# Kernel optimization log

Measured on AMD Instinct MI355X. Metric: run time of the kernel, lower is better.

The kernel has to match this reference:

```python
import jax, jax.numpy as jnp
import numpy as np

EMBED, PDIM, HEADS, FFN = 192, 96, 8, 384
HID = int(2 * FFN / 3)                        # 256
CH = [HID - (HID // 4) * 3] + [HID // 4] * 3  # [64, 64, 64, 64]
SCALES = [1, 3, 5, 7]
B, H, W = 8, 128, 128


def conv2d(x, w, b=None, pad=0, groups=1):
    out = jax.lax.conv_general_dilated(
        x, w, (1, 1), [(pad, pad), (pad, pad)],
        feature_group_count=groups,
        dimension_numbers=('NCHW', 'OIHW', 'NCHW'))
    return out if b is None else out + b[None, :, None, None]


def layer_norm(x, g, b, eps=1e-6):
    m = x.mean(-1, keepdims=True)
    v = ((x - m) ** 2).mean(-1, keepdims=True)
    return (x - m) * jax.lax.rsqrt(v + eps) * g + b


def batch_norm(x, g, b, m, v, eps=1e-5):
    # eval-mode BatchNorm2d with running stats
    inv = jax.lax.rsqrt(v + eps)
    return (x - m[None, :, None, None]) * (g * inv)[None, :, None, None] + b[None, :, None, None]


def block_forward(x, p):
    # --- pos: depthwise 3x3 residual ---
    xc = x.transpose(0, 3, 1, 2)  # NCHW
    xc = xc + conv2d(xc, p['pos_w'], p['pos_b'], pad=1, groups=EMBED)

    # --- retention (ATK_SPA) branch ---
    y = layer_norm(xc.transpose(0, 2, 3, 1), p['ln1_g'], p['ln1_b'])
    yc = y.transpose(0, 3, 1, 2)
    b, c, h, w = yc.shape
    x1, x2 = yc[:, :PDIM], yc[:, PDIM:]
    qkv = conv2d(conv2d(x1, p['qkv_w']), p['qkv_dw_w'], pad=1, groups=3 * PDIM)
    q, k, v = jnp.split(qkv, 3, axis=1)
    cph = PDIM // HEADS
    rs = lambda t: t.reshape(b, HEADS, cph, h * w)
    q, k, v = rs(q), rs(k), rs(v)
    q = q / jnp.maximum(jnp.linalg.norm(q, axis=-1, keepdims=True), 1e-12)
    k = k / jnp.maximum(jnp.linalg.norm(k, axis=-1, keepdims=True), 1e-12)
    attn = jnp.einsum('bhcn,bhdn->bhcd', q, k) * p['temperature']  # [b,heads,cph,cph]
    # dynamic top-k from gate (int() truncation -> floor, value is positive)
    g1 = jax.nn.relu(conv2d(yc, p['gate_w1'], p['gate_b1']))
    gate = jax.nn.sigmoid(conv2d(g1, p['gate_w2'], p['gate_b2']))
    dyn_k = jnp.floor(cph * gate.mean())
    # rank-based top-k mask == scatter of topk indices (jit-safe for dynamic k)
    ranks = jnp.argsort(jnp.argsort(-attn, axis=-1), axis=-1)
    mask = ranks.astype(attn.dtype) < dyn_k
    attn = jax.nn.softmax(jnp.where(mask, attn, -jnp.inf), axis=-1)
    out = jnp.einsum('bhcd,bhdn->bhcn', attn, v)
    # out1..out4 are identical; weighted sum == single matmul scaled
    out = out * (p['attn1'] + p['attn2'] + p['attn3'] + p['attn4'])
    out = out.reshape(b, PDIM, h, w)
    out = conv2d(jnp.concatenate([out, x2], axis=1), p['proj_w'])
    xc = xc + out

    # --- FFN (HSSFGN) branch ---
    z = layer_norm(xc.transpose(0, 2, 3, 1), p['ln2_g'], p['ln2_b'])
    zc = z.transpose(0, 3, 1, 2)
    v0 = batch_norm(jax.nn.gelu(conv2d(zc, p['fc1_w']), approximate=False),
                    p['bn1_g'], p['bn1_b'], p['bn1_m'], p['bn1_v'])
    parts = jnp.split(v0, np.cumsum(CH[:-1]).tolist(), axis=1)
    dws = [conv2d(parts[i], p['dw%d_w' % i], p['dw%d_b' % i],
                  pad=SCALES[i] // 2, groups=CH[i]) for i in range(4)]
    u = jnp.concatenate(dws, axis=1) + v0
    u = batch_norm(jax.nn.gelu(u, approximate=False),
                   p['bn2_g'], p['bn2_b'], p['bn2_m'], p['bn2_v'])
    u = u * v0
    u = batch_norm(conv2d(u, p['fc2_w']),
                   p['bn3_g'], p['bn3_b'], p['bn3_m'], p['bn3_v'])
    xc = xc + u
    return xc.transpose(0, 2, 3, 1)


def setup_inputs() -> dict:
    ki = iter(jax.random.split(jax.random.key(0), 64))
    nrm = lambda shape, s=0.05: jax.random.normal(next(ki), shape, dtype=jnp.float32) * s
    inp = {
        'x': jax.random.normal(next(ki), (B, H, W, EMBED), dtype=jnp.float32),
        'pos_w': nrm((EMBED, 1, 3, 3)), 'pos_b': jnp.zeros((EMBED,)),
        'ln1_g': jnp.ones((EMBED,)), 'ln1_b': jnp.zeros((EMBED,)),
        'temperature': jnp.ones((HEADS, 1, 1)),
        'qkv_w': nrm((3 * PDIM, PDIM, 1, 1)),
        'qkv_dw_w': nrm((3 * PDIM, 1, 3, 3)),
        'proj_w': nrm((EMBED, EMBED, 1, 1)),
        'gate_w1': nrm((EMBED // 2, EMBED, 1, 1), 0.02), 'gate_b1': jnp.zeros((EMBED // 2,)),
        'gate_w2': nrm((1, EMBED // 2, 1, 1), 0.02), 'gate_b2': jnp.zeros((1,)),
        'attn1': jnp.full((1,), 0.2), 'attn2': jnp.full((1,), 0.2),
        'attn3': jnp.full((1,), 0.2), 'attn4': jnp.full((1,), 0.2),
        'ln2_g': jnp.ones((EMBED,)), 'ln2_b': jnp.zeros((EMBED,)),
        'fc1_w': nrm((HID, EMBED, 1, 1)),
        'bn1_g': jnp.ones((HID,)), 'bn1_b': jnp.zeros((HID,)),
        'bn1_m': jnp.zeros((HID,)), 'bn1_v': jnp.ones((HID,)),
        'bn2_g': jnp.ones((HID,)), 'bn2_b': jnp.zeros((HID,)),
        'bn2_m': jnp.zeros((HID,)), 'bn2_v': jnp.ones((HID,)),
        'fc2_w': nrm((EMBED, HID, 1, 1)),
        'bn3_g': jnp.ones((EMBED,)), 'bn3_b': jnp.zeros((EMBED,)),
        'bn3_m': jnp.zeros((EMBED,)), 'bn3_v': jnp.ones((EMBED,)),
    }
    for i in range(4):
        inp['dw%d_w' % i] = nrm((CH[i], 1, SCALES[i], SCALES[i]))
        inp['dw%d_b' % i] = jnp.zeros((CH[i],))
    return inp


def reference(x, pos_w, pos_b, ln1_g, ln1_b, temperature, qkv_w, qkv_dw_w, proj_w,
              gate_w1, gate_b1, gate_w2, gate_b2, attn1, attn2, attn3, attn4,
              ln2_g, ln2_b, fc1_w, bn1_g, bn1_b, bn1_m, bn1_v,
              dw0_w, dw0_b, dw1_w, dw1_b, dw2_w, dw2_b, dw3_w, dw3_b,
              bn2_g, bn2_b, bn2_m, bn2_v, fc2_w, bn3_g, bn3_b, bn3_m, bn3_v):
    p = dict(locals())
    xx = p.pop('x')
    return block_forward(xx, p)
```

## Files before the change

kernel.cpp:

```cpp
#include <hip/hip_runtime.h>
#include <hip/hip_bf16.h>
#include <math.h>

#define BB 8
#define HH 128
#define WW 128
#define HW (HH*WW)
#define NPIX (BB*HW)

typedef unsigned short u16;
typedef __attribute__((ext_vector_type(4))) float  floatx4;
typedef __attribute__((ext_vector_type(4))) short  short4v;
typedef __attribute__((ext_vector_type(8))) short  short8v;

static __device__ __forceinline__ float gelu_exact(float x){
    return 0.5f*x*(1.0f+erff(x*0.70710678118654752440f));
}
static __device__ __forceinline__ float b2f(u16 v){
    union { unsigned u; float f; } x; x.u = ((unsigned)v)<<16; return x.f;
}
static __device__ __forceinline__ u16 f2b(float f){
    __hip_bfloat16 h = __float2bfloat16(f);
    return *(u16*)&h;
}

#define WQ 27648
#define WP 36864
#define WG 18432
#define WF1 49152
#define WF2 49152
#define WTOT (WQ+WP+WG+WF1+WF2)
__global__ __launch_bounds__(256) void wprep_k(const float* __restrict__ a,
    const float* __restrict__ b, const float* __restrict__ c,
    const float* __restrict__ d, const float* __restrict__ e, u16* __restrict__ o)
{
    int i = blockIdx.x*256 + threadIdx.x;
    if (i >= WTOT) return;
    float v;
    if (i < WQ) v = a[i];
    else if (i < WQ+WP) v = b[i-WQ];
    else if (i < WQ+WP+WG) v = c[i-WQ-WP];
    else if (i < WQ+WP+WG+WF1) v = d[i-WQ-WP-WG];
    else v = e[i-WQ-WP-WG-WF1];
    o[i] = f2b(v);
}

__global__ __launch_bounds__(256) void pos_conv_k(const float* __restrict__ x,
    const float* __restrict__ w, const float* __restrict__ bias, u16* __restrict__ out)
{
    int bid = blockIdx.x;
    int sb = (bid & 7)*(gridDim.x >> 3) + (bid >> 3);
    int gid = sb*256 + threadIdx.x;
    int c4 = gid % 48; int rest = gid / 48;
    int seg = rest & 15; rest >>= 4;
    int hy = rest % HH; int b = rest / HH;
    int c0 = c4*4;
    float wr[3][3][4];
    #pragma unroll
    for (int j=0;j<4;j++)
        #pragma unroll
        for (int ky=0;ky<3;ky++)
            #pragma unroll
            for (int kx=0;kx<3;kx++)
                wr[ky][kx][j] = w[(c0+j)*9 + ky*3 + kx];
    float4 bias4 = *(const float4*)(bias + c0);
    const float4* x4 = (const float4*)x;
    const float4* r0 = x4 + ((size_t)(b*HH + hy-1)*WW)*48 + c4;
    const float4* r1 = x4 + ((size_t)(b*HH + hy  )*WW)*48 + c4;
    const float4* r2 = x4 + ((size_t)(b*HH + hy+1)*WW)*48 + c4;
    bool v0 = hy > 0, v2 = hy < HH-1;
    float4 z4 = make_float4(0.f,0.f,0.f,0.f);
    int s0 = seg*8;
    float4 cA[3], cB[3], cC[3], cN[3];
    bool la = s0 > 0;
    cA[0] = (v0&&la) ? r0[(size_t)(s0-1)*48] : z4;
    cA[1] = la ? r1[(size_t)(s0-1)*48] : z4;
    cA[2] = (v2&&la) ? r2[(size_t)(s0-1)*48] : z4;
    cB[0] = v0 ? r0[(size_t)s0*48] : z4;  cB[1] = r1[(size_t)s0*48];  cB[2] = v2 ? r2[(size_t)s0*48] : z4;
    cC[0] = v0 ? r0[(size_t)(s0+1)*48] : z4; cC[1] = r1[(size_t)(s0+1)*48]; cC[2] = v2 ? r2[(size_t)(s0+1)*48] : z4;
    u16* orow = out + ((size_t)(b*HH + hy)*WW)*192 + c0;
    for (int i2=0; i2<8; i2++){
        int wx = s0 + i2;
        bool okc = (wx+2) < WW;
        size_t noff = (size_t)(wx+2)*48;
        cN[0] = (v0 && okc) ? r0[noff] : z4;
        cN[1] = okc ? r1[noff] : z4;
        cN[2] = (v2 && okc) ? r2[noff] : z4;
        float4 acc = bias4;
        #pragma unroll
        for (int i=0;i<3;i++){
            acc.x = fmaf(wr[i][0][0], cA[i].x, acc.x);
            acc.y = fmaf(wr[i][0][1], cA[i].y, acc.y);
            acc.z = fmaf(wr[i][0][2], cA[i].z, acc.z);
            acc.w = fmaf(wr[i][0][3], cA[i].w, acc.w);
            acc.x = fmaf(wr[i][1][0], cB[i].x, acc.x);
            acc.y = fmaf(wr[i][1][1], cB[i].y, acc.y);
            acc.z = fmaf(wr[i][1][2], cB[i].z, acc.z);
            acc.w = fmaf(wr[i][1][3], cB[i].w, acc.w);
            acc.x = fmaf(wr[i][2][0], cC[i].x, acc.x);
            acc.y = fmaf(wr[i][2][1], cC[i].y, acc.y);
            acc.z = fmaf(wr[i][2][2], cC[i].z, acc.z);
            acc.w = fmaf(wr[i][2][3], cC[i].w, acc.w);
        }
        acc.x += cB[1].x; acc.y += cB[1].y; acc.z += cB[1].z; acc.w += cB[1].w;
        short4v o; o.x=(short)f2b(acc.x); o.y=(short)f2b(acc.y);
        o.z=(short)f2b(acc.z); o.w=(short)f2b(acc.w);
        *(short4v*)(orow + (size_t)wx*192) = o;
        #pragma unroll
        for (int i=0;i<3;i++){ cA[i]=cB[i]; cB[i]=cC[i]; cC[i]=cN[i]; }
    }
}

__global__ __launch_bounds__(256) void ln_k(const u16* __restrict__ in,
    const float* __restrict__ g, const float* __restrict__ bta, u16* __restrict__ out)
{
    int wid = threadIdx.x >> 6, lane = threadIdx.x & 63;
    size_t pix = (size_t)blockIdx.x*4 + wid;
    const u16* row = in + pix*192;
    float x0 = b2f(row[lane]), x1 = b2f(row[lane+64]), x2 = b2f(row[lane+128]);
    float s = x0+x1+x2;
    float q = x0*x0 + x1*x1 + x2*x2;
    #pragma unroll
    for (int off=32; off; off>>=1){ s += __shfl_xor(s,off,64); q += __shfl_xor(q,off,64); }
    float mean = s*(1.f/192.f);
    float var  = q*(1.f/192.f) - mean*mean;
    float inv  = rsqrtf(var + 1e-6f);
    u16* orow = out + pix*192;
    orow[lane]     = f2b((x0-mean)*inv*g[lane]     + bta[lane]);
    orow[lane+64]  = f2b((x1-mean)*inv*g[lane+64]  + bta[lane+64]);
    orow[lane+128] = f2b((x2-mean)*inv*g[lane+128] + bta[lane+128]);
}

#define GM_NONE 0
#define GM_RES 1
#define GM_GELU_BN 2
#define GM_BN_RES 3
#define GM_BIAS_RELU 4
#define WSTR 264

template<int MODE, int K, bool SPLIT=false>
__global__ __launch_bounds__(256) void gemm_bf16_k(
    const u16* __restrict__ A, int lda,
    const u16* __restrict__ A2, int lda2,
    const u16* __restrict__ W,
    void* __restrict__ Cv, int ldc,
    const u16* __restrict__ R, int ldr,
    const float* __restrict__ bg, const float* __restrict__ bb,
    const float* __restrict__ bm_, const float* __restrict__ bv,
    int N)
{
    __shared__ u16 Ws[64*WSTR];
    int t = threadIdx.x;
    int bn = blockIdx.x * 64;
    int bm = blockIdx.y * 256;
    {
        constexpr int KQ = K/4;
        int brow = t >> 2, bq = t & 3;
        int n = bn + brow;
        bool nv = n < N;
        const u16* src = W + (size_t)n*K + bq*KQ;
        #pragma unroll
        for (int j=0; j<KQ; j+=8){
            short8v v = {};
            if (nv) v = *(const short8v*)(src + j);
            *(short8v*)&Ws[brow*WSTR + bq*KQ + j] = v;
        }
    }
    __syncthreads();
    int wave = t >> 6, lane = t & 63;
    int wm = wave*64;
    int lr = lane & 15, lk = lane >> 4;
    const u16* arow  = A + (size_t)(bm + wm + lr)*lda + lk*8;
    const u16* arow2 = SPLIT ? (A2 + (size_t)(bm + wm + lr)*lda2 + lk*8) : nullptr;
    floatx4 acc[4][4] = {};
    #pragma unroll
    for (int k0 = 0; k0 < K; k0 += 32){
        short8v afr[4];
        if (SPLIT && k0 >= 96){
            #pragma unroll
            for (int m=0;m<4;m++)
                afr[m] = *(const short8v*)(arow2 + (size_t)(m*16)*lda2 + (k0-96));
        } else {
            #pragma unroll
            for (int m=0;m<4;m++)
                afr[m] = *(const short8v*)(arow + (size_t)(m*16)*lda + k0);
        }
        #pragma unroll
        for (int n2=0;n2<4;n2++){
            short8v bfr = *(const short8v*)&Ws[(n2*16+lr)*WSTR + k0 + lk*8];
            #pragma unroll
            for (int m=0;m<4;m++)
                acc[m][n2] = __builtin_amdgcn_mfma_f32_16x16x32_bf16(afr[m], bfr, acc[m][n2], 0,0,0);
        }
    }
    #pragma unroll
    for (int m=0;m<4;m++){
        #pragma unroll
        for (int n2=0;n2<4;n2++){
            int gcol = bn + n2*16 + lr;
            if (gcol >= N) continue;
            #pragma unroll
            for (int rg=0; rg<4; rg++){
                int grow = bm + wm + m*16 + lk*4 + rg;
                float v = acc[m][n2][rg];
                if (MODE == GM_RES){
                    v += b2f(R[(size_t)grow*ldr + gcol]);
                    ((u16*)Cv)[(size_t)grow*ldc + gcol] = f2b(v);
                } else if (MODE == GM_BN_RES){
                    float bnv = (v - bm_[gcol])*rsqrtf(bv[gcol]+1e-5f)*bg[gcol] + bb[gcol];
                    ((float*)Cv)[(size_t)grow*ldc + gcol] = bnv + b2f(R[(size_t)grow*ldr + gcol]);
                } else if (MODE == GM_GELU_BN){
                    float gl = gelu_exact(v);
                    v = (gl - bm_[gcol])*rsqrtf(bv[gcol]+1e-5f)*bg[gcol] + bb[gcol];
                    ((u16*)Cv)[(size_t)grow*ldc + gcol] = f2b(v);
                } else if (MODE == GM_BIAS_RELU){
                    ((u16*)Cv)[(size_t)grow*ldc + gcol] = f2b(fmaxf(v + bg[gcol], 0.f));
                } else {
                    ((u16*)Cv)[(size_t)grow*ldc + gcol] = f2b(v);
                }
            }
        }
    }
}

__global__ __launch_bounds__(256) void gate2_k(const u16* __restrict__ G1,
    const float* __restrict__ w2, const float* __restrict__ b2, float* __restrict__ gpix)
{
    int pix = blockIdx.x*256 + threadIdx.x;
    const short4v* g4 = (const short4v*)(G1 + (size_t)pix*96);
    const float4* w4 = (const float4*)w2;
    float s = b2[0];
    #pragma unroll
    for (int j=0;j<24;j++){
        short4v g = g4[j]; float4 w = w4[j];
        s += b2f((u16)g.x)*w.x + b2f((u16)g.y)*w.y + b2f((u16)g.z)*w.z + b2f((u16)g.w)*w.w;
    }
    gpix[pix] = 1.f/(1.f+expf(-s));
}

__global__ __launch_bounds__(1024) void gate_reduce_k(const float* __restrict__ gpix,
                                                      float* __restrict__ dynk)
{
    __shared__ float sm[16];
    float s = 0.f;
    for (int i=threadIdx.x; i<NPIX; i+=1024) s += gpix[i];
    #pragma unroll
    for (int off=32; off; off>>=1) s += __shfl_xor(s,off,64);
    int wid = threadIdx.x>>6, lane = threadIdx.x&63;
    if (lane==0) sm[wid]=s;
    __syncthreads();
    if (threadIdx.x==0){
        float tot=0.f; for (int i=0;i<16;i++) tot+=sm[i];
        *dynk = floorf(12.0f * (tot/(float)NPIX));
    }
}

#define QPOS(c8) ((c8)*8 + ((c8)>>2)*4)
#define QTAPSTRIDE 324
__global__ __launch_bounds__(256) void qkv_dw_k(const u16* __restrict__ in,
    const float* __restrict__ w, u16* __restrict__ out)
{
    __shared__ float wlds[9*QTAPSTRIDE];
    int t = threadIdx.x;
    for (int i=t; i<2592; i+=256){
        int tap = i/288, cc = i%288;
        wlds[tap*QTAPSTRIDE + QPOS(cc>>3) + (cc&7)] = w[cc*9+tap];
    }
    __syncthreads();
    int bid = blockIdx.x;
    int sb = (bid & 7)*(gridDim.x >> 3) + (bid >> 3);
    int idx = sb*256 + t;
    int c8 = idx % 36; int px2 = idx / 36;
    int wp = px2 & 63; int hy = (px2 >> 6) & 127; int img = px2 >> 13;
    int wx0 = wp*2;
    int c0 = c8*8;
    int wofs = QPOS(c8);
    float acc0[8] = {}, acc1[8] = {};
    #pragma unroll
    for (int ky=0; ky<3; ky++){
        int hh = hy + ky - 1; if ((unsigned)hh >= HH) continue;
        const u16* rowp = in + ((size_t)(img*HH+hh)*WW)*288 + c0;
        #pragma unroll
        for (int cc=0; cc<4; cc++){
            int cx = wx0 - 1 + cc;
            if ((unsigned)cx >= WW) continue;
            short8v v = *(const short8v*)(rowp + (size_t)cx*288);
            float vf[8];
            #pragma unroll
            for (int j=0;j<8;j++) vf[j] = b2f((u16)v[j]);
            if (cc < 3){
                floatx4 wa = *(const floatx4*)&wlds[(ky*3+cc)*QTAPSTRIDE + wofs];
                floatx4 wb = *(const floatx4*)&wlds[(ky*3+cc)*QTAPSTRIDE + wofs + 4];
                #pragma unroll
                for (int j=0;j<4;j++){ acc0[j]   = fmaf(wa[j], vf[j],   acc0[j]);
                                       acc0[4+j] = fmaf(wb[j], vf[4+j], acc0[4+j]); }
            }
            if (cc >= 1){
                floatx4 wa = *(const floatx4*)&wlds[(ky*3+cc-1)*QTAPSTRIDE + wofs];
                floatx4 wb = *(const floatx4*)&wlds[(ky*3+cc-1)*QTAPSTRIDE + wofs + 4];
                #pragma unroll
                for (int j=0;j<4;j++){ acc1[j]   = fmaf(wa[j], vf[j],   acc1[j]);
                                       acc1[4+j] = fmaf(wb[j], vf[4+j], acc1[4+j]); }
            }
        }
    }
    size_t pix0 = (size_t)(img*HH+hy)*WW + wx0;
    short8v o0, o1;
    #pragma unroll
    for (int j=0;j<8;j++){ o0[j] = (short)f2b(acc0[j]); o1[j] = (short)f2b(acc1[j]); }
    *(short8v*)(out + pix0*288 + c0) = o0;
    *(short8v*)(out + (pix0+1)*288 + c0) = o1;
}

__global__ __launch_bounds__(256) void gram_k(const u16* __restrict__ QKVd,
                                              float* __restrict__ part)
{
    int bh = blockIdx.x;
    int slice = blockIdx.y;
    int img = bh >> 3, h = bh & 7;
    int qbase = h*12, kbase = 96 + h*12;
    const u16* base = QKVd + (size_t)img*HW*288;
    __shared__ float qs[64][12];
    __shared__ float ks[64][12];
    int t = threadIdx.x;
    float acc = 0.f;
    int c = (t<144) ? t/12 : (t<156 ? t-144 : t-156);
    int d = (t<144) ? t%12 : 0;
    for (int st=0; st<16; st++){
        int pix0 = slice*1024 + st*64;
        __syncthreads();
        for (int i=t; i<384; i+=256){
            int p = i/6, j = i%6;
            const u16* src = base + (size_t)(pix0+p)*288 + (j<3 ? qbase + j*4 : kbase + (j-3)*4);
            short4v v = *(const short4v*)src;
            float f0=b2f((u16)v.x), f1=b2f((u16)v.y), f2=b2f((u16)v.z), f3=b2f((u16)v.w);
            if (j<3){ int jj=j*4;     qs[p][jj]=f0; qs[p][jj+1]=f1; qs[p][jj+2]=f2; qs[p][jj+3]=f3; }
            else    { int jj=(j-3)*4; ks[p][jj]=f0; ks[p][jj+1]=f1; ks[p][jj+2]=f2; ks[p][jj+3]=f3; }
        }
        __syncthreads();
        if (t<144){        for (int p=0;p<64;p++) acc = fmaf(qs[p][c], ks[p][d], acc); }
        else if (t<156){   for (int p=0;p<64;p++) acc = fmaf(qs[p][c], qs[p][c], acc); }
        else if (t<168){   for (int p=0;p<64;p++) acc = fmaf(ks[p][c], ks[p][c], acc); }
    }
    if (t<168) part[((size_t)bh*16 + slice)*168 + t] = acc;
}

__global__ __launch_bounds__(256) void gram_combine_k(const float* __restrict__ part,
                                                      float* __restrict__ gram, int n)
{
    int i = blockIdx.x*256 + threadIdx.x;
    if (i >= n) return;
    int bh = i/168, t = i%168;
    float s = 0.f;
    for (int sl=0; sl<16; sl++) s += part[((size_t)bh*16+sl)*168 + t];
    gram[i] = s;
}

__global__ __launch_bounds__(256) void attn_k(const float* __restrict__ gram,
    const float* __restrict__ temp, const float* __restrict__ dynk_p,
    const float* __restrict__ a1, const float* __restrict__ a2,
    const float* __restrict__ a3, const float* __restrict__ a4,
    float* __restrict__ attnW)
{
    int bh = blockIdx.x;
    int h = bh & 7;
    __shared__ float av[12][12];
    __shared__ float mv[12][12];
    __shared__ float nq[12], nk[12];
    int t = threadIdx.x;
    if (t < 12) nq[t] = fmaxf(sqrtf(gram[bh*168+144+t]), 1e-12f);
    else if (t < 24) nk[t-12] = fmaxf(sqrtf(gram[bh*168+156+(t-12)]), 1e-12f);
    __syncthreads();
    if (t < 144){
        int c=t/12, d=t%12;
        av[c][d] = gram[bh*168+t] / (nq[c]*nk[d]) * temp[h];
    }
    __syncthreads();
    float dk = *dynk_p;
    if (t < 144){
        int c=t/12, d=t%12; float v = av[c][d];
        int r = 0;
        #pragma unroll
        for (int j=0;j<12;j++){
            float o = av[c][j];
            r += (o > v) ? 1 : ((o == v && j < d) ? 1 : 0);
        }
        mv[c][d] = ((float)r < dk) ? v : -INFINITY;
    }
    __syncthreads();
    if (t < 12){
        float mx = -INFINITY;
        for (int d2=0; d2<12; d2++) mx = fmaxf(mx, mv[t][d2]);
        float e[12]; float s = 0.f;
        for (int d2=0; d2<12; d2++){ e[d2] = expf(mv[t][d2]-mx); s += e[d2]; }
        float sc = (a1[0]+a2[0]+a3[0]+a4[0]) / s;
        for (int d2=0; d2<12; d2++) attnW[(size_t)bh*144 + t*12 + d2] = e[d2]*sc;
    }
}

__global__ __launch_bounds__(256) void attn_apply_k(const u16* __restrict__ QKVd,
    const float* __restrict__ attnW, u16* __restrict__ P)
{
    int gid = blockIdx.x*256 + threadIdx.x;
    int h = gid % 8; size_t pix = (size_t)(gid / 8);
    int img = (int)(pix >> 14);
    const u16* vp = QKVd + pix*288 + 192 + h*12;
    float vf[12];
    #pragma unroll
    for (int j=0;j<3;j++){
        short4v v = *(const short4v*)(vp + j*4);
        vf[j*4+0]=b2f((u16)v.x); vf[j*4+1]=b2f((u16)v.y);
        vf[j*4+2]=b2f((u16)v.z); vf[j*4+3]=b2f((u16)v.w);
    }
    const float* awb = attnW + ((size_t)(img*8+h))*144;
    u16 o[12];
    #pragma unroll
    for (int cc=0; cc<12; cc++){
        const float4* ap = (const float4*)(awb + cc*12);
        float4 a0 = ap[0], a1 = ap[1], a2 = ap[2];
        float s = a0.x*vf[0] + a0.y*vf[1] + a0.z*vf[2] + a0.w*vf[3]
                + a1.x*vf[4] + a1.y*vf[5] + a1.z*vf[6] + a1.w*vf[7]
                + a2.x*vf[8] + a2.y*vf[9] + a2.z*vf[10]+ a2.w*vf[11];
        o[cc] = f2b(s);
    }
    u16* op = P + pix*96 + h*12;
    *(short4v*)(op)   = *(short4v*)&o[0];
    *(short4v*)(op+4) = *(short4v*)&o[4];
    *(short4v*)(op+8) = *(short4v*)&o[8];
}

template<int KS>
__global__ __launch_bounds__(256) void ffn_dw_g(const u16* __restrict__ V0,
    const float* __restrict__ wsrc, const float* __restrict__ bsrc, int cbase,
    const float* __restrict__ bn2g, const float* __restrict__ bn2b,
    const float* __restrict__ bn2m, const float* __restrict__ bn2v,
    u16* __restrict__ U)
{
    constexpr int PAD = KS/2;
    __shared__ float wlds[KS*KS*64];
    __shared__ float bng[64], bnb[64], bnm[64], bnvr[64];
    int t = threadIdx.x;
    for (int i=t; i<KS*KS*64; i+=256){
        int tap = i >> 6, cc = i & 63;
        wlds[tap*64 + cc] = wsrc[cc*KS*KS + tap];
    }
    if (t < 64){
        bng[t] = bn2g[cbase+t]; bnb[t] = bn2b[cbase+t];
        bnm[t] = bn2m[cbase+t]; bnvr[t] = rsqrtf(bn2v[cbase+t]+1e-5f);
    }
    __syncthreads();
    int ci = t & 7, seg = t >> 3;
    int bid = blockIdx.x;
    int rowid = (bid & 7)*(gridDim.x >> 3) + (bid >> 3);
    int img = rowid >> 7, hy = rowid & 127;
    int c0r = ci*8;
    int c0 = cbase + c0r;
    int x0 = seg*4;
    float acc[4][8];
    {
        floatx4 b0 = *(const floatx4*)(bsrc + c0r);
        floatx4 b1 = *(const floatx4*)(bsrc + c0r + 4);
        #pragma unroll
        for (int dx=0;dx<4;dx++){
            #pragma unroll
            for (int j=0;j<4;j++){ acc[dx][j]=b0[j]; acc[dx][4+j]=b1[j]; }
        }
    }
    #pragma unroll
    for (int ky=0; ky<KS; ky++){
        int hh = hy + ky - PAD;
        if ((unsigned)hh >= HH) continue;
        float wr[KS][8];
        #pragma unroll
        for (int kx=0; kx<KS; kx++){
            floatx4 wa = *(const floatx4*)&wlds[(ky*KS+kx)*64 + c0r];
            floatx4 wb = *(const floatx4*)&wlds[(ky*KS+kx)*64 + c0r + 4];
            #pragma unroll
            for (int j=0;j<4;j++){ wr[kx][j]=wa[j]; wr[kx][4+j]=wb[j]; }
        }
        const u16* rowp = V0 + ((size_t)(img*HH+hh)*WW)*256 + c0;
        #pragma unroll
        for (int cc=0; cc<4+2*PAD; cc++){
            int cx = x0 - PAD + cc;
            if ((unsigned)cx >= WW) continue;
            short8v v = *(const short8v*)(rowp + (size_t)cx*256);
            float vf[8];
            #pragma unroll
            for (int j=0;j<8;j++) vf[j] = b2f((u16)v[j]);
            #pragma unroll
            for (int dx=0; dx<4; dx++){
                int kx = cc - dx;
                if (kx < 0 || kx >= KS) continue;
                #pragma unroll
                for (int j=0;j<8;j++) acc[dx][j] = fmaf(wr[kx][j], vf[j], acc[dx][j]);
            }
        }
    }
    size_t rbase = (size_t)(img*HH+hy)*WW;
    #pragma unroll
    for (int dx=0; dx<4; dx++){
        size_t pix = rbase + x0 + dx;
        short8v vc = *(const short8v*)(V0 + pix*256 + c0);
        short8v o;
        #pragma unroll
        for (int j=0;j<8;j++){
            float v0c = b2f((u16)vc[j]);
            float u1 = acc[dx][j] + v0c;
            float gl = gelu_exact(u1);
            float bn = (gl - bnm[c0r+j])*bnvr[c0r+j]*bng[c0r+j] + bnb[c0r+j];
            o[j] = (short)f2b(bn*v0c);
        }
        *(short8v*)(U + pix*256 + c0) = o;
    }
}

extern "C" void kernel_launch(void* const* d_in, const int* in_sizes, int n_in,
                              void* d_out, int out_size, void* d_ws, size_t ws_size,
                              hipStream_t stream)
{
    const float* x     = (const float*)d_in[0];
    const float* pos_w = (const float*)d_in[1];
    const float* pos_b = (const float*)d_in[2];
    const float* ln1g  = (const float*)d_in[3];
    const float* ln1b  = (const float*)d_in[4];
    const float* temp  = (const float*)d_in[5];
    const float* qkvw  = (const float*)d_in[6];
    const float* qkvdw = (const float*)d_in[7];
    const float* projw = (const float*)d_in[8];
    const float* gw1   = (const float*)d_in[9];
    const float* gb1   = (const float*)d_in[10];
    const float* gw2   = (const float*)d_in[11];
    const float* gb2   = (const float*)d_in[12];
    const float* a1    = (const float*)d_in[13];
    const float* a2    = (const float*)d_in[14];
    const float* a3    = (const float*)d_in[15];
    const float* a4    = (const float*)d_in[16];
    const float* ln2g  = (const float*)d_in[17];
    const float* ln2b  = (const float*)d_in[18];
    const float* fc1w  = (const float*)d_in[19];
    const float* bn1g  = (const float*)d_in[20];
    const float* bn1b  = (const float*)d_in[21];
    const float* bn1m  = (const float*)d_in[22];
    const float* bn1v  = (const float*)d_in[23];
    const float* bn2g  = (const float*)d_in[24];
    const float* bn2b  = (const float*)d_in[25];
    const float* bn2m  = (const float*)d_in[26];
    const float* bn2v  = (const float*)d_in[27];
    const float* fc2w  = (const float*)d_in[28];
    const float* bn3g  = (const float*)d_in[29];
    const float* bn3b  = (const float*)d_in[30];
    const float* bn3m  = (const float*)d_in[31];
    const float* bn3v  = (const float*)d_in[32];
    const float* dw0w  = (const float*)d_in[33];
    const float* dw0b  = (const float*)d_in[34];
    const float* dw1w  = (const float*)d_in[35];
    const float* dw1b  = (const float*)d_in[36];
    const float* dw2w  = (const float*)d_in[37];
    const float* dw2b  = (const float*)d_in[38];
    const float* dw3w  = (const float*)d_in[39];
    const float* dw3b  = (const float*)d_in[40];

    float* OUT = (float*)d_out;

    char* p = (char*)d_ws;
    float* gpix  = (float*)p;                 p += (size_t)NPIX*4;
    float* dynk  = (float*)p;                 p += 256;
    float* gpart = (float*)p;                 p += 64*16*168*4;
    float* gram  = (float*)p;                 p += 64*168*4;
    float* attnW = (float*)p;                 p += 64*144*4;
    u16*   wbf   = (u16*)p;                   p += (size_t)WTOT*2;
    u16*   Abf   = (u16*)p;                   p += (size_t)NPIX*192*2;
    size_t fixedB = (size_t)(p - (char*)d_ws);

    size_t perImg = (size_t)HW*2*(192+288+288);
    int CBr = 2;
    if (ws_size >= fixedB + 8*perImg) CBr = 8;
    else if (ws_size >= fixedB + 4*perImg) CBr = 4;
    int NCHUNKr = BB/CBr;
    size_t CHWr = (size_t)CBr*HW;

    u16* Ybf = (u16*)p;                   p += CHWr*192*2;
    u16* B1  = (u16*)p;                   p += CHWr*288*2;
    u16* B2  = (u16*)p;
    u16* qkvwb = wbf;
    u16* projwb= wbf + WQ;
    u16* gw1b  = wbf + WQ + WP;
    u16* fc1b  = wbf + WQ + WP + WG;
    u16* fc2b  = wbf + WQ + WP + WG + WF1;
    u16* G1bf  = B1;
    u16* QKVbf = B1;
    u16* QKVdbf= B2;
    u16* P96   = B1;
    u16* Zbf   = B2;
    u16* V0bf  = B1;
    u16* Ubf   = B2;

    wprep_k<<<(WTOT+255)/256, 256, 0, stream>>>(qkvw, projw, gw1, fc1w, fc2w, wbf);
    pos_conv_k<<<BB*HH*16*48/256, 256, 0, stream>>>(x, pos_w, pos_b, Abf);

    for (int c=0; c<NCHUNKr; c++){
        const u16* Ab = Abf + (size_t)c*CHWr*192;
        ln_k<<<CHWr/4, 256, 0, stream>>>(Ab, ln1g, ln1b, Ybf);
        dim3 g(2, CHWr/256);
        gemm_bf16_k<GM_BIAS_RELU,192><<<g, 256, 0, stream>>>(Ybf, 192, nullptr, 0,
            gw1b, G1bf, 96, nullptr, 0, gb1, nullptr, nullptr, nullptr, 96);
        gate2_k<<<CHWr/256, 256, 0, stream>>>(G1bf, gw2, gb2, gpix + (size_t)c*CHWr);
    }
    gate_reduce_k<<<1, 1024, 0, stream>>>(gpix, dynk);

    for (int c=0; c<NCHUNKr; c++){
        u16* Ab = Abf + (size_t)c*CHWr*192;
        if (NCHUNKr > 1)
            ln_k<<<CHWr/4, 256, 0, stream>>>(Ab, ln1g, ln1b, Ybf);
        {
            dim3 g(5, CHWr/256);
            gemm_bf16_k<GM_NONE,96><<<g, 256, 0, stream>>>(Ybf, 192, nullptr, 0,
                qkvwb, QKVbf, 288, nullptr, 0, nullptr,nullptr,nullptr,nullptr, 288);
        }
        qkv_dw_k<<<CHWr*18/256, 256, 0, stream>>>(QKVbf, qkvdw, QKVdbf);
        { dim3 g(CBr*8, 16); gram_k<<<g, 256, 0, stream>>>(QKVdbf, gpart); }
        gram_combine_k<<<(CBr*8*168+255)/256, 256, 0, stream>>>(gpart, gram, CBr*8*168);
        attn_k<<<CBr*8, 256, 0, stream>>>(gram, temp, dynk, a1,a2,a3,a4, attnW);
        attn_apply_k<<<CHWr*8/256, 256, 0, stream>>>(QKVdbf, attnW, P96);
        {
            dim3 g(3, CHWr/256);
            gemm_bf16_k<GM_RES,192,true><<<g, 256, 0, stream>>>(P96, 96, Ybf+96, 192,
                projwb, Ab, 192, Ab, 192, nullptr,nullptr,nullptr,nullptr, 192);
        }
        ln_k<<<CHWr/4, 256, 0, stream>>>(Ab, ln2g, ln2b, Zbf);
        {
            dim3 g(4, CHWr/256);
            gemm_bf16_k<GM_GELU_BN,192><<<g, 256, 0, stream>>>(Zbf, 192, nullptr, 0,
                fc1b, V0bf, 256, nullptr, 0, bn1g,bn1b,bn1m,bn1v, 256);
        }
        int rows = (int)(CHWr/WW);
        ffn_dw_g<1><<<rows, 256, 0, stream>>>(V0bf, dw0w, dw0b, 0,
            bn2g,bn2b,bn2m,bn2v, Ubf);
        ffn_dw_g<3><<<rows, 256, 0, stream>>>(V0bf, dw1w, dw1b, 64,
            bn2g,bn2b,bn2m,bn2v, Ubf);
        ffn_dw_g<5><<<rows, 256, 0, stream>>>(V0bf, dw2w, dw2b, 128,
            bn2g,bn2b,bn2m,bn2v, Ubf);
        ffn_dw_g<7><<<rows, 256, 0, stream>>>(V0bf, dw3w, dw3b, 192,
            bn2g,bn2b,bn2m,bn2v, Ubf);
        {
            dim3 g(3, CHWr/256);
            gemm_bf16_k<GM_BN_RES,256><<<g, 256, 0, stream>>>(Ubf, 256, nullptr, 0,
                fc2b, OUT + (size_t)c*CHWr*192, 192, Ab, 192, bn3g,bn3b,bn3m,bn3v, 192);
        }
    }
}
```

Measured before the change: 655.5 us.

## Split depthwise QKV output into separate Q, K, V planes and prefetch deeper in pos conv

The depthwise QKV kernel now writes Q, K and V into three separate planes of 96 channels each instead of one interleaved 288-channel buffer. The gram and attention-apply kernels read only the plane they need, so their reads touch fewer cache lines per pixel. Separately, the positional depthwise conv loads one extra column ahead, a deeper register prefetch, at the cost of more live registers.

```diff
diff --git a/kernel.cpp b/kernel.cpp
--- a/kernel.cpp
+++ b/kernel.cpp
@@ -71,18 +71,25 @@
     bool v0 = hy > 0, v2 = hy < HH-1;
     float4 z4 = make_float4(0.f,0.f,0.f,0.f);
     int s0 = seg*8;
-    float4 cA[3], cB[3], cC[3], cN[3];
+    float4 cA[3], cB[3], cC[3], cP[3], cN[3];
     bool la = s0 > 0;
     cA[0] = (v0&&la) ? r0[(size_t)(s0-1)*48] : z4;
     cA[1] = la ? r1[(size_t)(s0-1)*48] : z4;
     cA[2] = (v2&&la) ? r2[(size_t)(s0-1)*48] : z4;
     cB[0] = v0 ? r0[(size_t)s0*48] : z4;  cB[1] = r1[(size_t)s0*48];  cB[2] = v2 ? r2[(size_t)s0*48] : z4;
     cC[0] = v0 ? r0[(size_t)(s0+1)*48] : z4; cC[1] = r1[(size_t)(s0+1)*48]; cC[2] = v2 ? r2[(size_t)(s0+1)*48] : z4;
+    {
+        bool ok = (s0+2) < WW;
+        size_t off = (size_t)(s0+2)*48;
+        cP[0] = (v0&&ok) ? r0[off] : z4;
+        cP[1] = ok ? r1[off] : z4;
+        cP[2] = (v2&&ok) ? r2[off] : z4;
+    }
     u16* orow = out + ((size_t)(b*HH + hy)*WW)*192 + c0;
     for (int i2=0; i2<8; i2++){
         int wx = s0 + i2;
-        bool okc = (wx+2) < WW;
-        size_t noff = (size_t)(wx+2)*48;
+        bool okc = (wx+3) < WW;
+        size_t noff = (size_t)(wx+3)*48;
         cN[0] = (v0 && okc) ? r0[noff] : z4;
         cN[1] = okc ? r1[noff] : z4;
         cN[2] = (v2 && okc) ? r2[noff] : z4;
@@ -107,7 +114,7 @@
         o.z=(short)f2b(acc.z); o.w=(short)f2b(acc.w);
         *(short4v*)(orow + (size_t)wx*192) = o;
         #pragma unroll
-        for (int i=0;i<3;i++){ cA[i]=cB[i]; cB[i]=cC[i]; cC[i]=cN[i]; }
+        for (int i=0;i<3;i++){ cA[i]=cB[i]; cB[i]=cC[i]; cC[i]=cP[i]; cP[i]=cN[i]; }
     }
 }
 
@@ -258,7 +265,7 @@
 #define QPOS(c8) ((c8)*8 + ((c8)>>2)*4)
 #define QTAPSTRIDE 324
 __global__ __launch_bounds__(256) void qkv_dw_k(const u16* __restrict__ in,
-    const float* __restrict__ w, u16* __restrict__ out)
+    const float* __restrict__ w, u16* __restrict__ out, size_t planeStride)
 {
     __shared__ float wlds[9*QTAPSTRIDE];
     int t = threadIdx.x;
@@ -305,21 +312,23 @@
         }
     }
     size_t pix0 = (size_t)(img*HH+hy)*WW + wx0;
+    int sec = c0/96, qc0 = c0 - sec*96;
+    u16* outp = out + (size_t)sec*planeStride + qc0;
     short8v o0, o1;
     #pragma unroll
     for (int j=0;j<8;j++){ o0[j] = (short)f2b(acc0[j]); o1[j] = (short)f2b(acc1[j]); }
-    *(short8v*)(out + pix0*288 + c0) = o0;
-    *(short8v*)(out + (pix0+1)*288 + c0) = o1;
-}
-
-__global__ __launch_bounds__(256) void gram_k(const u16* __restrict__ QKVd,
-                                              float* __restrict__ part)
+    *(short8v*)(outp + pix0*96) = o0;
+    *(short8v*)(outp + (pix0+1)*96) = o1;
+}
+
+__global__ __launch_bounds__(256) void gram_k(const u16* __restrict__ Qp,
+    const u16* __restrict__ Kp, float* __restrict__ part)
 {
     int bh = blockIdx.x;
     int slice = blockIdx.y;
     int img = bh >> 3, h = bh & 7;
-    int qbase = h*12, kbase = 96 + h*12;
-    const u16* base = QKVd + (size_t)img*HW*288;
+    const u16* Qb = Qp + (size_t)img*HW*96 + h*12;
+    const u16* Kb = Kp + (size_t)img*HW*96 + h*12;
     __shared__ float qs[64][12];
     __shared__ float ks[64][12];
     int t = threadIdx.x;
@@ -331,7 +340,8 @@
         __syncthreads();
         for (int i=t; i<384; i+=256){
             int p = i/6, j = i%6;
-            const u16* src = base + (size_t)(pix0+p)*288 + (j<3 ? qbase + j*4 : kbase + (j-3)*4);
+            const u16* src = (j<3) ? (Qb + (size_t)(pix0+p)*96 + j*4)
+                                   : (Kb + (size_t)(pix0+p)*96 + (j-3)*4);
             short4v v = *(const short4v*)src;
             float f0=b2f((u16)v.x), f1=b2f((u16)v.y), f2=b2f((u16)v.z), f3=b2f((u16)v.w);
             if (j<3){ int jj=j*4;     qs[p][jj]=f0; qs[p][jj+1]=f1; qs[p][jj+2]=f2; qs[p][jj+3]=f3; }
@@ -398,13 +408,13 @@
     }
 }
 
-__global__ __launch_bounds__(256) void attn_apply_k(const u16* __restrict__ QKVd,
+__global__ __launch_bounds__(256) void attn_apply_k(const u16* __restrict__ Vp,
     const float* __restrict__ attnW, u16* __restrict__ P)
 {
     int gid = blockIdx.x*256 + threadIdx.x;
     int h = gid % 8; size_t pix = (size_t)(gid / 8);
     int img = (int)(pix >> 14);
-    const u16* vp = QKVd + pix*288 + 192 + h*12;
+    const u16* vp = Vp + pix*96 + h*12;
     float vf[12];
     #pragma unroll
     for (int j=0;j<3;j++){
@@ -617,11 +627,12 @@
             gemm_bf16_k<GM_NONE,96><<<g, 256, 0, stream>>>(Ybf, 192, nullptr, 0,
                 qkvwb, QKVbf, 288, nullptr, 0, nullptr,nullptr,nullptr,nullptr, 288);
         }
-        qkv_dw_k<<<CHWr*18/256, 256, 0, stream>>>(QKVbf, qkvdw, QKVdbf);
-        { dim3 g(CBr*8, 16); gram_k<<<g, 256, 0, stream>>>(QKVdbf, gpart); }
+        size_t pstr = CHWr*96;
+        qkv_dw_k<<<CHWr*18/256, 256, 0, stream>>>(QKVbf, qkvdw, QKVdbf, pstr);
+        { dim3 g(CBr*8, 16); gram_k<<<g, 256, 0, stream>>>(QKVdbf, QKVdbf + pstr, gpart); }
         gram_combine_k<<<(CBr*8*168+255)/256, 256, 0, stream>>>(gpart, gram, CBr*8*168);
         attn_k<<<CBr*8, 256, 0, stream>>>(gram, temp, dynk, a1,a2,a3,a4, attnW);
-        attn_apply_k<<<CHWr*8/256, 256, 0, stream>>>(QKVdbf, attnW, P96);
+        attn_apply_k<<<CHWr*8/256, 256, 0, stream>>>(QKVdbf + 2*pstr, attnW, P96);
         {
             dim3 g(3, CHWr/256);
             gemm_bf16_k<GM_RES,192,true><<<g, 256, 0, stream>>>(P96, 96, Ybf+96, 192,
```

Result: no change. 655.0 us (-0.1%).
